# Kernel tuning notes

Hardware: AMD Instinct MI355X
Metric: run time of the kernel (lower is better)

Reference implementation:

```python
import jax, jax.numpy as jnp
import numpy as np

N_NODES = 100000
N_EDGES = 1600000
IN_DIM = 7
HID = 64
OUT_DIM = 1
EPS = 1e-5  # BatchNorm1d eps


def setup_inputs() -> dict:
    key = jax.random.key(0)
    ks = jax.random.split(key, 16)
    x = jax.random.normal(ks[0], (N_NODES, IN_DIM), dtype=jnp.float32)
    edge_index = jax.random.randint(ks[1], (2, N_EDGES), 0, N_NODES)

    def lin(k, din, dout):
        # Glorot-ish init for a [din, dout] weight (x @ W convention)
        return jax.random.normal(k, (din, dout), dtype=jnp.float32) / np.float32(np.sqrt(din))

    inp = {"x": x, "edge_index": edge_index}
    dims = [(IN_DIM, HID), (HID, HID), (HID, HID)]
    i = 2
    for l, (din, dout) in enumerate(dims):
        inp[f"Wl{l}"] = lin(ks[i], din, dout); i += 1   # SAGEConv lin_l (applied to aggregated neighbors), carries bias
        inp[f"bl{l}"] = jnp.zeros((dout,), jnp.float32)
        inp[f"Wr{l}"] = lin(ks[i], din, dout); i += 1   # SAGEConv lin_r (root/self weight, no bias)
        inp[f"g{l}"] = jnp.ones((dout,), jnp.float32)   # BN gamma
        inp[f"be{l}"] = jnp.zeros((dout,), jnp.float32) # BN beta
    inp["Wo"] = lin(ks[i], HID, OUT_DIM); i += 1
    inp["bo"] = jnp.zeros((OUT_DIM,), jnp.float32)
    return inp


def _sage_bn_relu(x, src, dst, Wl, bl, Wr, g, be):
    # SAGEConv(aggr='mean'): out = lin_l(mean_{j->i} x_j) + lin_r(x_i)
    n = x.shape[0]
    msg = x[src]                                               # [E, d] gather
    s = jax.ops.segment_sum(msg, dst, num_segments=n)          # [N, d] scatter-add
    cnt = jax.ops.segment_sum(jnp.ones((src.shape[0],), x.dtype), dst, num_segments=n)
    agg = s / jnp.maximum(cnt, 1.0)[:, None]                   # scatter-mean (isolated nodes -> 0)
    h = agg @ Wl + bl + x @ Wr
    # BatchNorm1d (training-mode batch statistics over nodes)
    mu = h.mean(axis=0)
    var = h.var(axis=0)
    h = g * (h - mu) * jax.lax.rsqrt(var + EPS) + be
    return jax.nn.relu(h)


def reference(x, edge_index, Wl0, bl0, Wr0, g0, be0, Wl1, bl1, Wr1, g1, be1, Wl2, bl2, Wr2, g2, be2, Wo, bo):
    src, dst = edge_index[0], edge_index[1]
    h = _sage_bn_relu(x, src, dst, Wl0, bl0, Wr0, g0, be0)
    h = _sage_bn_relu(h, src, dst, Wl1, bl1, Wr1, g1, be1)
    h = _sage_bn_relu(h, src, dst, Wl2, bl2, Wr2, g2, be2)
    return h @ Wo + bo                                         # [N, 1]
```

## Files before the change

### kernel.cpp

```cpp
#include <hip/hip_runtime.h>

#define EPSV 1e-5f
#define REP 8
#define SBCAP 1280
#define CWIN 16640

static __device__ __forceinline__ ushort f2bf(float f) {
    unsigned u = __float_as_uint(f);
    unsigned r = (u + 0x7FFF + ((u >> 16) & 1)) >> 16;
    return (ushort)r;
}


__global__ __launch_bounds__(256) void sb_scatter(
    const int* __restrict__ src, const int* __restrict__ dst,
    int* __restrict__ sbcnt, int* __restrict__ bbuf, int E, int NSB)
{
    __shared__ int hist[512];
    __shared__ int gbase[512];
    int t = threadIdx.x;
    int r = blockIdx.x & (REP - 1);
    for (int i = t; i < NSB; i += 256) hist[i] = 0;
    __syncthreads();

    int base_i = (blockIdx.x * 256 + t) * 8;
    int d[8], s[8], rk[8];
    int m = E - base_i; m = m < 0 ? 0 : (m > 8 ? 8 : m);
    if (m == 8) {
        int4 da = *reinterpret_cast<const int4*>(dst + base_i);
        int4 db = *reinterpret_cast<const int4*>(dst + base_i + 4);
        int4 sa = *reinterpret_cast<const int4*>(src + base_i);
        int4 sb4 = *reinterpret_cast<const int4*>(src + base_i + 4);
        d[0] = da.x; d[1] = da.y; d[2] = da.z; d[3] = da.w;
        d[4] = db.x; d[5] = db.y; d[6] = db.z; d[7] = db.w;
        s[0] = sa.x; s[1] = sa.y; s[2] = sa.z; s[3] = sa.w;
        s[4] = sb4.x; s[5] = sb4.y; s[6] = sb4.z; s[7] = sb4.w;
    } else {
        for (int k = 0; k < m; ++k) { d[k] = dst[base_i + k]; s[k] = src[base_i + k]; }
    }
    for (int k = 0; k < m; ++k)
        rk[k] = atomicAdd(&hist[d[k] >> 9], 1);
    __syncthreads();

    for (int i = t; i < NSB; i += 256) {
        int c = hist[i];
        gbase[i] = c ? atomicAdd(&sbcnt[(r * NSB + i) * 16], c) : 0;
    }
    __syncthreads();

    for (int k = 0; k < m; ++k) {
        int sbk = d[k] >> 9;
        int pos = gbase[sbk] + rk[k];
        if (pos < SBCAP)
            bbuf[(size_t)(r * NSB + sbk) * SBCAP + pos] = ((d[k] & 511) << 17) | s[k];
    }
}

__global__ __launch_bounds__(512) void sb_build(
    const int* __restrict__ sbcnt, const int* __restrict__ bbuf,
    int2* __restrict__ seg, int* __restrict__ col, int n, int NSB)
{
    __shared__ int cnt[512], off[512], cur[512];
    int sb = blockIdx.x;
    int node0 = sb << 9;
    int t = threadIdx.x;
    cnt[t] = 0;
    __syncthreads();

    for (int r = 0; r < REP; ++r) {
        int c = min(sbcnt[(r * NSB + sb) * 16], SBCAP);
        const int* __restrict__ w = bbuf + (size_t)(r * NSB + sb) * SBCAP;
        for (int i = t; i < c; i += 512) atomicAdd(&cnt[w[i] >> 17], 1);
    }
    __syncthreads();

    if (t < 64) {
        int v[8]; int run = 0;
#pragma unroll
        for (int k = 0; k < 8; ++k) {
            v[k] = run;
            run += (cnt[t * 8 + k] + 15) & ~15;
        }
        int pre = run;
        for (int dd = 1; dd < 64; dd <<= 1) {
            int tm = __shfl_up(pre, dd);
            if (t >= dd) pre += tm;
        }
        int lane_excl = pre - run;
#pragma unroll
        for (int k = 0; k < 8; ++k) off[t * 8 + k] = lane_excl + v[k];
    }
    __syncthreads();

    int colbase = sb * CWIN;
    {
        int node = node0 + t;
        if (node < n) seg[node] = make_int2(colbase + off[t], cnt[t]);
        cur[t] = off[t];
    }
    __syncthreads();

    for (int r = 0; r < REP; ++r) {
        int c = min(sbcnt[(r * NSB + sb) * 16], SBCAP);
        const int* __restrict__ w = bbuf + (size_t)(r * NSB + sb) * SBCAP;
        for (int i = t; i < c; i += 512) {
            int e = w[i];
            int p = atomicAdd(&cur[e >> 17], 1);
            col[colbase + p] = e & 0x1FFFF;
        }
    }
    __syncthreads();
    {
        int pend = off[t] + ((cnt[t] + 15) & ~15);
        for (int p = off[t] + cnt[t]; p < pend; ++p) col[colbase + p] = n;
    }
}


__global__ __launch_bounds__(512) void transform7(
    const float* __restrict__ x,
    const float* __restrict__ Wl, const float* __restrict__ bl, const float* __restrict__ Wr,
    ushort* __restrict__ yl, float* __restrict__ h, int n)
{
    __shared__ float swl[7 * 64], swr[7 * 64], sbl[64];
    for (int i = threadIdx.x; i < 7 * 64; i += 512) { swl[i] = Wl[i]; swr[i] = Wr[i]; }
    if (threadIdx.x < 64) sbl[threadIdx.x] = bl[threadIdx.x];
    __syncthreads();

    if (blockIdx.x == 0 && threadIdx.x < 64) yl[(size_t)n * 64 + threadIdx.x] = 0;

    int lane = threadIdx.x & 63;
    int node = blockIdx.x * 8 + (threadIdx.x >> 6);
    if (node >= n) return;

    float xv = (lane < 7) ? x[(size_t)node * 7 + lane] : 0.f;
    float hl = 0.f, hr = sbl[lane];
#pragma unroll
    for (int k = 0; k < 7; ++k) {
        float xk = __shfl(xv, k);
        hl += xk * swl[k * 64 + lane];
        hr += xk * swr[k * 64 + lane];
    }
    yl[(size_t)node * 64 + lane] = f2bf(hl);
    h[(size_t)node * 64 + lane] = hr;
}


__global__ __launch_bounds__(256) void transform64(
    const float* __restrict__ zin, const float* __restrict__ scale, const float* __restrict__ shift,
    const float* __restrict__ Wl, const float* __restrict__ Wr, const float* __restrict__ bl,
    ushort* __restrict__ yl, float* __restrict__ h, int n)
{
    __shared__ float zt[64][68];
    __shared__ float swl[64 * 64];
    __shared__ float swr[64 * 64];
    __shared__ float ssc[64], ssh[64], sbl[64];

    int t = threadIdx.x;
    if (t < 64) { ssc[t] = scale[t]; ssh[t] = shift[t]; sbl[t] = bl[t]; }
    for (int i = t; i < 4096; i += 256) { swl[i] = Wl[i]; swr[i] = Wr[i]; }
    __syncthreads();

    int node0 = blockIdx.x * 64;
    {
        int m = t >> 2, c4 = (t & 3) * 16;
        int gm = node0 + m;
        if (gm < n) {
            const float4* zp = reinterpret_cast<const float4*>(zin + (size_t)gm * 64 + c4);
#pragma unroll
            for (int j = 0; j < 4; ++j) {
                float4 v = zp[j];
                int c = c4 + j * 4;
                v.x = fmaxf(v.x * ssc[c + 0] + ssh[c + 0], 0.f);
                v.y = fmaxf(v.y * ssc[c + 1] + ssh[c + 1], 0.f);
                v.z = fmaxf(v.z * ssc[c + 2] + ssh[c + 2], 0.f);
                v.w = fmaxf(v.w * ssc[c + 3] + ssh[c + 3], 0.f);
                zt[m][c + 0] = v.x; zt[m][c + 1] = v.y; zt[m][c + 2] = v.z; zt[m][c + 3] = v.w;
            }
        } else {
#pragma unroll
            for (int j = 0; j < 16; ++j) zt[m][c4 + j] = 0.f;
        }
    }
    __syncthreads();

    int ng = t >> 4;
    int cg = t & 15;
    int mb = ng * 4;
    const float* sw = (cg < 8) ? swl : swr;
    int c0 = (cg & 7) * 8;

    float acc[4][8];
#pragma unroll
    for (int i = 0; i < 4; ++i)
#pragma unroll
        for (int j = 0; j < 8; ++j) acc[i][j] = 0.f;

#pragma unroll 4
    for (int k = 0; k < 64; ++k) {
        float z0 = zt[mb + 0][k];
        float z1 = zt[mb + 1][k];
        float z2 = zt[mb + 2][k];
        float z3 = zt[mb + 3][k];
        float4 wa = *reinterpret_cast<const float4*>(sw + k * 64 + c0);
        float4 wb = *reinterpret_cast<const float4*>(sw + k * 64 + c0 + 4);
        float w[8] = {wa.x, wa.y, wa.z, wa.w, wb.x, wb.y, wb.z, wb.w};
#pragma unroll
        for (int j = 0; j < 8; ++j) {
            acc[0][j] += z0 * w[j];
            acc[1][j] += z1 * w[j];
            acc[2][j] += z2 * w[j];
            acc[3][j] += z3 * w[j];
        }
    }

#pragma unroll
    for (int i = 0; i < 4; ++i) {
        int gm = node0 + mb + i;
        if (gm >= n) continue;
        if (cg < 8) {
            uint4 pk;
            pk.x = (unsigned)f2bf(acc[i][0]) | ((unsigned)f2bf(acc[i][1]) << 16);
            pk.y = (unsigned)f2bf(acc[i][2]) | ((unsigned)f2bf(acc[i][3]) << 16);
            pk.z = (unsigned)f2bf(acc[i][4]) | ((unsigned)f2bf(acc[i][5]) << 16);
            pk.w = (unsigned)f2bf(acc[i][6]) | ((unsigned)f2bf(acc[i][7]) << 16);
            *reinterpret_cast<uint4*>(yl + (size_t)gm * 64 + c0) = pk;
        } else {
            float* dp = h + (size_t)gm * 64 + c0;
            *reinterpret_cast<float4*>(dp) =
                make_float4(acc[i][0] + sbl[c0 + 0], acc[i][1] + sbl[c0 + 1],
                            acc[i][2] + sbl[c0 + 2], acc[i][3] + sbl[c0 + 3]);
            *reinterpret_cast<float4*>(dp + 4) =
                make_float4(acc[i][4] + sbl[c0 + 4], acc[i][5] + sbl[c0 + 5],
                            acc[i][6] + sbl[c0 + 6], acc[i][7] + sbl[c0 + 7]);
        }
    }
}


__global__ __launch_bounds__(512) void gather_kernel(
    const ushort* __restrict__ yl, float* __restrict__ h,
    const int* __restrict__ col, const int2* __restrict__ seg,
    float* __restrict__ sums, int n)
{
    __shared__ float ls[128];
    int t = threadIdx.x;
    if (t < 128) ls[t] = 0.f;
    __syncthreads();

    int lane = t & 63;
    int g = lane >> 3, s = lane & 7;
    const unsigned* __restrict__ ylu = reinterpret_cast<const unsigned*>(yl);

    float ss0 = 0.f, ss1 = 0.f, ss2 = 0.f, ss3 = 0.f;
    float sq0 = 0.f, sq1 = 0.f, sq2 = 0.f, sq3 = 0.f;

    int nw = gridDim.x * 8;
    for (int node = blockIdx.x * 8 + (t >> 6); node < n; node += nw) {
        int2 sc = seg[node];
        int s0  = __builtin_amdgcn_readfirstlane(sc.x);
        int deg = __builtin_amdgcn_readfirstlane(sc.y);
        int pc  = (deg + 15) & ~15;
        const int* __restrict__ cp = col + s0;

        float a0 = 0.f, a1 = 0.f, a2 = 0.f, a3 = 0.f;
        float a4 = 0.f, a5 = 0.f, a6 = 0.f, a7 = 0.f;
        for (int j0 = 0; j0 < pc; j0 += 16) {
            int i0 = cp[j0 + g];
            int i1 = cp[j0 + 8 + g];
            uint4 ua = *reinterpret_cast<const uint4*>(ylu + ((size_t)i0 << 5) + s * 4);
            uint4 ub = *reinterpret_cast<const uint4*>(ylu + ((size_t)i1 << 5) + s * 4);
            a0 += __uint_as_float(ua.x << 16);        a1 += __uint_as_float(ua.x & 0xFFFF0000u);
            a2 += __uint_as_float(ua.y << 16);        a3 += __uint_as_float(ua.y & 0xFFFF0000u);
            a4 += __uint_as_float(ua.z << 16);        a5 += __uint_as_float(ua.z & 0xFFFF0000u);
            a6 += __uint_as_float(ua.w << 16);        a7 += __uint_as_float(ua.w & 0xFFFF0000u);
            a0 += __uint_as_float(ub.x << 16);        a1 += __uint_as_float(ub.x & 0xFFFF0000u);
            a2 += __uint_as_float(ub.y << 16);        a3 += __uint_as_float(ub.y & 0xFFFF0000u);
            a4 += __uint_as_float(ub.z << 16);        a5 += __uint_as_float(ub.z & 0xFFFF0000u);
            a6 += __uint_as_float(ub.w << 16);        a7 += __uint_as_float(ub.w & 0xFFFF0000u);
        }
#pragma unroll
        for (int mk = 8; mk <= 32; mk <<= 1) {
            a0 += __shfl_xor(a0, mk); a1 += __shfl_xor(a1, mk);
            a2 += __shfl_xor(a2, mk); a3 += __shfl_xor(a3, mk);
            a4 += __shfl_xor(a4, mk); a5 += __shfl_xor(a5, mk);
            a6 += __shfl_xor(a6, mk); a7 += __shfl_xor(a7, mk);
        }
        if (g < 2) {
            float inv = 1.f / (float)max(deg, 1);
            float b0 = (g ? a4 : a0), b1 = (g ? a5 : a1), b2 = (g ? a6 : a2), b3 = (g ? a7 : a3);
            float* hp = h + (size_t)node * 64 + s * 8 + g * 4;
            float4 hv = *reinterpret_cast<float4*>(hp);
            hv.x += b0 * inv; hv.y += b1 * inv; hv.z += b2 * inv; hv.w += b3 * inv;
            *reinterpret_cast<float4*>(hp) = hv;
            ss0 += hv.x; sq0 += hv.x * hv.x;
            ss1 += hv.y; sq1 += hv.y * hv.y;
            ss2 += hv.z; sq2 += hv.z * hv.z;
            ss3 += hv.w; sq3 += hv.w * hv.w;
        }
    }
    if (g < 2) {
        int cb = s * 8 + g * 4;
        atomicAdd(&ls[cb + 0], ss0); atomicAdd(&ls[cb + 1], ss1);
        atomicAdd(&ls[cb + 2], ss2); atomicAdd(&ls[cb + 3], ss3);
        atomicAdd(&ls[64 + cb + 0], sq0); atomicAdd(&ls[64 + cb + 1], sq1);
        atomicAdd(&ls[64 + cb + 2], sq2); atomicAdd(&ls[64 + cb + 3], sq3);
    }
    __syncthreads();
    if (t < 128) atomicAdd(&sums[t], ls[t]);
}

__global__ void bn_finalize(const float* __restrict__ sums, const float* __restrict__ g,
                            const float* __restrict__ be, float* __restrict__ scale,
                            float* __restrict__ shift, int n) {
    int c = threadIdx.x;
    if (c < 64) {
        float inv_n = 1.f / (float)n;
        float mu = sums[c] * inv_n;
        float var = sums[64 + c] * inv_n - mu * mu;
        float sc = g[c] * rsqrtf(var + EPSV);
        scale[c] = sc;
        shift[c] = be[c] - mu * sc;
    }
}


__global__ __launch_bounds__(256) void out_kernel(const float* __restrict__ h,
                                                  const float* __restrict__ scale,
                                                  const float* __restrict__ shift,
                                                  const float* __restrict__ Wo,
                                                  const float* __restrict__ bo,
                                                  float* __restrict__ out, int n) {
    int lane = threadIdx.x & 63;
    int wave = threadIdx.x >> 6;
    int node = blockIdx.x * 4 + wave;
    if (node >= n) return;
    float v = h[(size_t)node * 64 + lane];
    v = fmaxf(v * scale[lane] + shift[lane], 0.f);
    float p = v * Wo[lane];
    for (int d = 32; d > 0; d >>= 1) p += __shfl_xor(p, d);
    if (lane == 0) out[node] = p + bo[0];
}


extern "C" void kernel_launch(void* const* d_in, const int* in_sizes, int n_in,
                              void* d_out, int out_size, void* d_ws, size_t ws_size,
                              hipStream_t stream) {
    const float* x   = (const float*)d_in[0];
    const int*   ei  = (const int*)d_in[1];
    const float* Wl0 = (const float*)d_in[2];
    const float* bl0 = (const float*)d_in[3];
    const float* Wr0 = (const float*)d_in[4];
    const float* g0  = (const float*)d_in[5];
    const float* be0 = (const float*)d_in[6];
    const float* Wl1 = (const float*)d_in[7];
    const float* bl1 = (const float*)d_in[8];
    const float* Wr1 = (const float*)d_in[9];
    const float* g1  = (const float*)d_in[10];
    const float* be1 = (const float*)d_in[11];
    const float* Wl2 = (const float*)d_in[12];
    const float* bl2 = (const float*)d_in[13];
    const float* Wr2 = (const float*)d_in[14];
    const float* g2  = (const float*)d_in[15];
    const float* be2 = (const float*)d_in[16];
    const float* Wo  = (const float*)d_in[17];
    const float* bo  = (const float*)d_in[18];

    const int N = in_sizes[0] / 7;
    const int E = in_sizes[1] / 2;
    const int NSB = (N + 511) / 512;
    const int* srcp = ei;
    const int* dstp = ei + E;

    char* ws = (char*)d_ws;
    size_t off = 0;
    auto walloc = [&](size_t bytes) -> void* {
        void* p = ws + off;
        off = (off + bytes + 255) & ~(size_t)255;
        return p;
    };
    int*    sbcnt  = (int*)walloc((size_t)REP * NSB * 16 * sizeof(int));
    int*    bbuf   = (int*)walloc((size_t)REP * NSB * SBCAP * sizeof(int));
    int2*   seg    = (int2*)walloc((size_t)(N + 1) * sizeof(int2));
    int*    col    = (int*)walloc((size_t)NSB * CWIN * sizeof(int));
    float*  sums   = (float*)walloc(3 * 128 * sizeof(float));
    float*  scale  = (float*)walloc(3 * 64 * sizeof(float));
    float*  shift  = (float*)walloc(3 * 64 * sizeof(float));
    ushort* yl     = (ushort*)walloc(((size_t)N + 1) * 64 * sizeof(ushort));
    float*  h0     = (float*)walloc((size_t)N * 64 * sizeof(float));
    float*  h1     = (float*)walloc((size_t)N * 64 * sizeof(float));

    hipMemsetAsync(sbcnt, 0, (size_t)REP * NSB * 16 * sizeof(int), stream);
    hipMemsetAsync(sums, 0, 3 * 128 * sizeof(float), stream);

    sb_scatter<<<(E + 2047) / 2048, 256, 0, stream>>>(srcp, dstp, sbcnt, bbuf, E, NSB);
    sb_build<<<NSB, 512, 0, stream>>>(sbcnt, bbuf, seg, col, N, NSB);

    const int gw  = (N + 7) / 8;
    const int gp  = 1024;
    const int gt  = (N + 63) / 64;

    transform7<<<gw, 512, 0, stream>>>(x, Wl0, bl0, Wr0, yl, h0, N);
    gather_kernel<<<gp, 512, 0, stream>>>(yl, h0, col, seg, sums, N);
    bn_finalize<<<1, 64, 0, stream>>>(sums, g0, be0, scale, shift, N);

    transform64<<<gt, 256, 0, stream>>>(h0, scale, shift, Wl1, Wr1, bl1, yl, h1, N);
    gather_kernel<<<gp, 512, 0, stream>>>(yl, h1, col, seg, sums + 128, N);
    bn_finalize<<<1, 64, 0, stream>>>(sums + 128, g1, be1, scale + 64, shift + 64, N);

    transform64<<<gt, 256, 0, stream>>>(h1, scale + 64, shift + 64, Wl2, Wr2, bl2, yl, h0, N);
    gather_kernel<<<gp, 512, 0, stream>>>(yl, h0, col, seg, sums + 256, N);
    bn_finalize<<<1, 64, 0, stream>>>(sums + 256, g2, be2, scale + 128, shift + 128, N);

    out_kernel<<<(N + 3) / 4, 256, 0, stream>>>(h0, scale + 128, shift + 128, Wo, bo, (float*)d_out, N);
}
```

Baseline: 323.8 us.

## Fuse BN finalize into consumers and gather two nodes per wave

```diff
diff --git a/kernel.cpp b/kernel.cpp
--- a/kernel.cpp
+++ b/kernel.cpp
@@ -147,7 +147,8 @@
 
 
 __global__ __launch_bounds__(256) void transform64(
-    const float* __restrict__ zin, const float* __restrict__ scale, const float* __restrict__ shift,
+    const float* __restrict__ zin, const float* __restrict__ sums,
+    const float* __restrict__ g, const float* __restrict__ be,
     const float* __restrict__ Wl, const float* __restrict__ Wr, const float* __restrict__ bl,
     ushort* __restrict__ yl, float* __restrict__ h, int n)
 {
@@ -157,7 +158,15 @@
     __shared__ float ssc[64], ssh[64], sbl[64];
 
     int t = threadIdx.x;
-    if (t < 64) { ssc[t] = scale[t]; ssh[t] = shift[t]; sbl[t] = bl[t]; }
+    if (t < 64) {
+        float inv_n = 1.f / (float)n;
+        float mu = sums[t] * inv_n;
+        float var = sums[64 + t] * inv_n - mu * mu;
+        float sc = g[t] * rsqrtf(var + EPSV);
+        ssc[t] = sc;
+        ssh[t] = be[t] - mu * sc;
+        sbl[t] = bl[t];
+    }
     for (int i = t; i < 4096; i += 256) { swl[i] = Wl[i]; swr[i] = Wr[i]; }
     __syncthreads();
 
@@ -256,28 +265,56 @@
     float sq0 = 0.f, sq1 = 0.f, sq2 = 0.f, sq3 = 0.f;
 
     int nw = gridDim.x * 8;
-    for (int node = blockIdx.x * 8 + (t >> 6); node < n; node += nw) {
-        int2 sc = seg[node];
-        int s0  = __builtin_amdgcn_readfirstlane(sc.x);
-        int deg = __builtin_amdgcn_readfirstlane(sc.y);
-        int pc  = (deg + 15) & ~15;
-        const int* __restrict__ cp = col + s0;
+    for (int n0 = blockIdx.x * 8 + (t >> 6); n0 < n; n0 += 2 * nw) {
+        int n1 = n0 + nw;
+        int2 sc0 = seg[n0];
+        int s0  = __builtin_amdgcn_readfirstlane(sc0.x);
+        int d0  = __builtin_amdgcn_readfirstlane(sc0.y);
+        int s1 = 0, d1 = 0;
+        if (n1 < n) {
+            int2 sc1 = seg[n1];
+            s1 = __builtin_amdgcn_readfirstlane(sc1.x);
+            d1 = __builtin_amdgcn_readfirstlane(sc1.y);
+        }
+        int pc0 = (d0 + 15) & ~15;
+        int pc1 = (d1 + 15) & ~15;
+        int pcm = max(pc0, pc1);
+        const int* __restrict__ cp0 = col + s0;
+        const int* __restrict__ cp1 = col + s1;
 
         float a0 = 0.f, a1 = 0.f, a2 = 0.f, a3 = 0.f;
         float a4 = 0.f, a5 = 0.f, a6 = 0.f, a7 = 0.f;
-        for (int j0 = 0; j0 < pc; j0 += 16) {
-            int i0 = cp[j0 + g];
-            int i1 = cp[j0 + 8 + g];
-            uint4 ua = *reinterpret_cast<const uint4*>(ylu + ((size_t)i0 << 5) + s * 4);
-            uint4 ub = *reinterpret_cast<const uint4*>(ylu + ((size_t)i1 << 5) + s * 4);
-            a0 += __uint_as_float(ua.x << 16);        a1 += __uint_as_float(ua.x & 0xFFFF0000u);
-            a2 += __uint_as_float(ua.y << 16);        a3 += __uint_as_float(ua.y & 0xFFFF0000u);
-            a4 += __uint_as_float(ua.z << 16);        a5 += __uint_as_float(ua.z & 0xFFFF0000u);
-            a6 += __uint_as_float(ua.w << 16);        a7 += __uint_as_float(ua.w & 0xFFFF0000u);
-            a0 += __uint_as_float(ub.x << 16);        a1 += __uint_as_float(ub.x & 0xFFFF0000u);
-            a2 += __uint_as_float(ub.y << 16);        a3 += __uint_as_float(ub.y & 0xFFFF0000u);
-            a4 += __uint_as_float(ub.z << 16);        a5 += __uint_as_float(ub.z & 0xFFFF0000u);
-            a6 += __uint_as_float(ub.w << 16);        a7 += __uint_as_float(ub.w & 0xFFFF0000u);
+        float b0 = 0.f, b1 = 0.f, b2 = 0.f, b3 = 0.f;
+        float b4 = 0.f, b5 = 0.f, b6 = 0.f, b7 = 0.f;
+        for (int j0 = 0; j0 < pcm; j0 += 16) {
+            if (j0 < pc0) {
+                int i0 = cp0[j0 + g];
+                int i1 = cp0[j0 + 8 + g];
+                uint4 ua = *reinterpret_cast<const uint4*>(ylu + ((size_t)i0 << 5) + s * 4);
+                uint4 ub = *reinterpret_cast<const uint4*>(ylu + ((size_t)i1 << 5) + s * 4);
+                a0 += __uint_as_float(ua.x << 16);    a1 += __uint_as_float(ua.x & 0xFFFF0000u);
+                a2 += __uint_as_float(ua.y << 16);    a3 += __uint_as_float(ua.y & 0xFFFF0000u);
+                a4 += __uint_as_float(ua.z << 16);    a5 += __uint_as_float(ua.z & 0xFFFF0000u);
+                a6 += __uint_as_float(ua.w << 16);    a7 += __uint_as_float(ua.w & 0xFFFF0000u);
+                a0 += __uint_as_float(ub.x << 16);    a1 += __uint_as_float(ub.x & 0xFFFF0000u);
+                a2 += __uint_as_float(ub.y << 16);    a3 += __uint_as_float(ub.y & 0xFFFF0000u);
+                a4 += __uint_as_float(ub.z << 16);    a5 += __uint_as_float(ub.z & 0xFFFF0000u);
+                a6 += __uint_as_float(ub.w << 16);    a7 += __uint_as_float(ub.w & 0xFFFF0000u);
+            }
+            if (j0 < pc1) {
+                int i0 = cp1[j0 + g];
+                int i1 = cp1[j0 + 8 + g];
+                uint4 ua = *reinterpret_cast<const uint4*>(ylu + ((size_t)i0 << 5) + s * 4);
+                uint4 ub = *reinterpret_cast<const uint4*>(ylu + ((size_t)i1 << 5) + s * 4);
+                b0 += __uint_as_float(ua.x << 16);    b1 += __uint_as_float(ua.x & 0xFFFF0000u);
+                b2 += __uint_as_float(ua.y << 16);    b3 += __uint_as_float(ua.y & 0xFFFF0000u);
+                b4 += __uint_as_float(ua.z << 16);    b5 += __uint_as_float(ua.z & 0xFFFF0000u);
+                b6 += __uint_as_float(ua.w << 16);    b7 += __uint_as_float(ua.w & 0xFFFF0000u);
+                b0 += __uint_as_float(ub.x << 16);    b1 += __uint_as_float(ub.x & 0xFFFF0000u);
+                b2 += __uint_as_float(ub.y << 16);    b3 += __uint_as_float(ub.y & 0xFFFF0000u);
+                b4 += __uint_as_float(ub.z << 16);    b5 += __uint_as_float(ub.z & 0xFFFF0000u);
+                b6 += __uint_as_float(ub.w << 16);    b7 += __uint_as_float(ub.w & 0xFFFF0000u);
+            }
         }
 #pragma unroll
         for (int mk = 8; mk <= 32; mk <<= 1) {
@@ -285,22 +322,38 @@
             a2 += __shfl_xor(a2, mk); a3 += __shfl_xor(a3, mk);
             a4 += __shfl_xor(a4, mk); a5 += __shfl_xor(a5, mk);
             a6 += __shfl_xor(a6, mk); a7 += __shfl_xor(a7, mk);
+            b0 += __shfl_xor(b0, mk); b1 += __shfl_xor(b1, mk);
+            b2 += __shfl_xor(b2, mk); b3 += __shfl_xor(b3, mk);
+            b4 += __shfl_xor(b4, mk); b5 += __shfl_xor(b5, mk);
+            b6 += __shfl_xor(b6, mk); b7 += __shfl_xor(b7, mk);
         }
         if (g < 2) {
-            float inv = 1.f / (float)max(deg, 1);
-            float b0 = (g ? a4 : a0), b1 = (g ? a5 : a1), b2 = (g ? a6 : a2), b3 = (g ? a7 : a3);
-            float* hp = h + (size_t)node * 64 + s * 8 + g * 4;
+            float inv = 1.f / (float)max(d0, 1);
+            float c0 = (g ? a4 : a0), c1 = (g ? a5 : a1), c2 = (g ? a6 : a2), c3 = (g ? a7 : a3);
+            float* hp = h + (size_t)n0 * 64 + s * 8 + g * 4;
             float4 hv = *reinterpret_cast<float4*>(hp);
-            hv.x += b0 * inv; hv.y += b1 * inv; hv.z += b2 * inv; hv.w += b3 * inv;
+            hv.x += c0 * inv; hv.y += c1 * inv; hv.z += c2 * inv; hv.w += c3 * inv;
             *reinterpret_cast<float4*>(hp) = hv;
             ss0 += hv.x; sq0 += hv.x * hv.x;
             ss1 += hv.y; sq1 += hv.y * hv.y;
             ss2 += hv.z; sq2 += hv.z * hv.z;
             ss3 += hv.w; sq3 += hv.w * hv.w;
-        }
-    }
-    if (g < 2) {
-        int cb = s * 8 + g * 4;
+        } else if (g < 4 && n1 < n) {
+            int gg = g - 2;
+            float inv = 1.f / (float)max(d1, 1);
+            float c0 = (gg ? b4 : b0), c1 = (gg ? b5 : b1), c2 = (gg ? b6 : b2), c3 = (gg ? b7 : b3);
+            float* hp = h + (size_t)n1 * 64 + s * 8 + gg * 4;
+            float4 hv = *reinterpret_cast<float4*>(hp);
+            hv.x += c0 * inv; hv.y += c1 * inv; hv.z += c2 * inv; hv.w += c3 * inv;
+            *reinterpret_cast<float4*>(hp) = hv;
+            ss0 += hv.x; sq0 += hv.x * hv.x;
+            ss1 += hv.y; sq1 += hv.y * hv.y;
+            ss2 += hv.z; sq2 += hv.z * hv.z;
+            ss3 += hv.w; sq3 += hv.w * hv.w;
+        }
+    }
+    {
+        int cb = s * 8 + ((g == 1 || g == 3) ? 4 : 0);
         atomicAdd(&ls[cb + 0], ss0); atomicAdd(&ls[cb + 1], ss1);
         atomicAdd(&ls[cb + 2], ss2); atomicAdd(&ls[cb + 3], ss3);
         atomicAdd(&ls[64 + cb + 0], sq0); atomicAdd(&ls[64 + cb + 1], sq1);
@@ -310,33 +363,31 @@
     if (t < 128) atomicAdd(&sums[t], ls[t]);
 }
 
-__global__ void bn_finalize(const float* __restrict__ sums, const float* __restrict__ g,
-                            const float* __restrict__ be, float* __restrict__ scale,
-                            float* __restrict__ shift, int n) {
-    int c = threadIdx.x;
-    if (c < 64) {
-        float inv_n = 1.f / (float)n;
-        float mu = sums[c] * inv_n;
-        float var = sums[64 + c] * inv_n - mu * mu;
-        float sc = g[c] * rsqrtf(var + EPSV);
-        scale[c] = sc;
-        shift[c] = be[c] - mu * sc;
-    }
-}
-
 
 __global__ __launch_bounds__(256) void out_kernel(const float* __restrict__ h,
-                                                  const float* __restrict__ scale,
-                                                  const float* __restrict__ shift,
+                                                  const float* __restrict__ sums,
+                                                  const float* __restrict__ g,
+                                                  const float* __restrict__ be,
                                                   const float* __restrict__ Wo,
                                                   const float* __restrict__ bo,
                                                   float* __restrict__ out, int n) {
-    int lane = threadIdx.x & 63;
-    int wave = threadIdx.x >> 6;
+    __shared__ float ssc[64], ssh[64];
+    int t = threadIdx.x;
+    if (t < 64) {
+        float inv_n = 1.f / (float)n;
+        float mu = sums[t] * inv_n;
+        float var = sums[64 + t] * inv_n - mu * mu;
+        float sc = g[t] * rsqrtf(var + EPSV);
+        ssc[t] = sc;
+        ssh[t] = be[t] - mu * sc;
+    }
+    __syncthreads();
+    int lane = t & 63;
+    int wave = t >> 6;
     int node = blockIdx.x * 4 + wave;
     if (node >= n) return;
     float v = h[(size_t)node * 64 + lane];
-    v = fmaxf(v * scale[lane] + shift[lane], 0.f);
+    v = fmaxf(v * ssc[lane] + ssh[lane], 0.f);
     float p = v * Wo[lane];
     for (int d = 32; d > 0; d >>= 1) p += __shfl_xor(p, d);
     if (lane == 0) out[node] = p + bo[0];
@@ -384,8 +435,6 @@
     int2*   seg    = (int2*)walloc((size_t)(N + 1) * sizeof(int2));
     int*    col    = (int*)walloc((size_t)NSB * CWIN * sizeof(int));
     float*  sums   = (float*)walloc(3 * 128 * sizeof(float));
-    float*  scale  = (float*)walloc(3 * 64 * sizeof(float));
-    float*  shift  = (float*)walloc(3 * 64 * sizeof(float));
     ushort* yl     = (ushort*)walloc(((size_t)N + 1) * 64 * sizeof(ushort));
     float*  h0     = (float*)walloc((size_t)N * 64 * sizeof(float));
     float*  h1     = (float*)walloc((size_t)N * 64 * sizeof(float));
@@ -402,15 +451,12 @@
 
     transform7<<<gw, 512, 0, stream>>>(x, Wl0, bl0, Wr0, yl, h0, N);
     gather_kernel<<<gp, 512, 0, stream>>>(yl, h0, col, seg, sums, N);
-    bn_finalize<<<1, 64, 0, stream>>>(sums, g0, be0, scale, shift, N);
-
-    transform64<<<gt, 256, 0, stream>>>(h0, scale, shift, Wl1, Wr1, bl1, yl, h1, N);
+
+    transform64<<<gt, 256, 0, stream>>>(h0, sums, g0, be0, Wl1, Wr1, bl1, yl, h1, N);
     gather_kernel<<<gp, 512, 0, stream>>>(yl, h1, col, seg, sums + 128, N);
-    bn_finalize<<<1, 64, 0, stream>>>(sums + 128, g1, be1, scale + 64, shift + 64, N);
-
-    transform64<<<gt, 256, 0, stream>>>(h1, scale + 64, shift + 64, Wl2, Wr2, bl2, yl, h0, N);
+
+    transform64<<<gt, 256, 0, stream>>>(h1, sums + 128, g1, be1, Wl2, Wr2, bl2, yl, h0, N);
     gather_kernel<<<gp, 512, 0, stream>>>(yl, h0, col, seg, sums + 256, N);
-    bn_finalize<<<1, 64, 0, stream>>>(sums + 256, g2, be2, scale + 128, shift + 128, N);
-
-    out_kernel<<<(N + 3) / 4, 256, 0, stream>>>(h0, scale + 128, shift + 128, Wo, bo, (float*)d_out, N);
-}
+
+    out_kernel<<<(N + 3) / 4, 256, 0, stream>>>(h0, sums + 256, g2, be2, Wo, bo, (float*)d_out, N);
+}
```

Measured after the change: 402.2 us. +24.2%, slower.
